# Kernel optimization log

Hardware: AMD Instinct MI355X
Metric: run time of the kernel (lower is better)

## Reference

```python
import jax, jax.numpy as jnp
import numpy as np

N_NODES = 100000
N_EDGES = 1000000
N_GRAPHS = 512
IN_DIM = 3
HID = 64


def setup_inputs() -> dict:
    key = jax.random.key(0)
    ks = jax.random.split(key, 7)
    x = jax.random.normal(ks[0], (N_NODES, IN_DIM), dtype=jnp.float32)
    edge_index = jax.random.randint(ks[1], (2, N_EDGES), 0, N_NODES, dtype=jnp.int64)
    batch = jnp.sort(jax.random.randint(ks[2], (N_NODES,), 0, N_GRAPHS, dtype=jnp.int64))
    # Glorot-ish init for GCNConv linear weights (PyG uses glorot), zero bias.
    W1 = jax.random.normal(ks[3], (IN_DIM, HID), dtype=jnp.float32) / np.float32(np.sqrt(IN_DIM))
    b1 = jnp.zeros((HID,), dtype=jnp.float32)
    W2 = jax.random.normal(ks[4], (HID, HID), dtype=jnp.float32) / np.float32(np.sqrt(HID))
    b2 = jnp.zeros((HID,), dtype=jnp.float32)
    return {"x": x, "W1": W1, "b1": b1, "W2": W2, "b2": b2,
            "edge_index": edge_index, "batch": batch}


def reference(x, W1, b1, W2, b2, edge_index, batch):
    n = x.shape[0]
    loop = jnp.arange(n)
    # GCNConv adds self-loops, then symmetric normalization D^-1/2 (A+I) D^-1/2
    src = jnp.concatenate([edge_index[0], loop])  # [E+N]
    dst = jnp.concatenate([edge_index[1], loop])  # [E+N]
    deg = jax.ops.segment_sum(jnp.ones(dst.shape[0], x.dtype), dst, num_segments=n)
    dinv = jnp.where(deg > 0, jax.lax.rsqrt(deg), 0.0)
    norm = dinv[src] * dinv[dst]  # [E+N]

    def gcn_conv(h, W, b):
        hw = h @ W                       # [N, out] linear first (PyG order)
        msg = hw[src] * norm[:, None]    # gather + scale, [E+N, out]
        agg = jax.ops.segment_sum(msg, dst, num_segments=n)  # scatter-add
        return agg + b

    h = jax.nn.relu(gcn_conv(x, W1, b1))
    h = jax.nn.relu(gcn_conv(h, W2, b2))

    # global_mean_pool over the batch vector
    sums = jax.ops.segment_sum(h, batch, num_segments=N_GRAPHS)          # [G, HID]
    counts = jax.ops.segment_sum(jnp.ones(n, h.dtype), batch, num_segments=N_GRAPHS)
    return sums / jnp.maximum(counts, 1.0)[:, None]
```

## Files before the change

kernel.cpp:

```cpp
#include <hip/hip_runtime.h>

#define HID 64
#define N_GRAPHS_C 512
#define BSHIFT 8
#define NBUCK_MAX 512
#define CAP 3264
#define EPB 4096

typedef unsigned short u16;
typedef unsigned int u32;
typedef unsigned long long u64;

__device__ __forceinline__ float bf2f(u16 u) {
    union { u32 i; float f; } v; v.i = ((u32)u) << 16; return v.f;
}
__device__ __forceinline__ u16 f2bf(float f) {
    union { float f; u32 i; } v; v.f = f;
    u32 x = v.i;
    return (u16)((x + 0x7fffu + ((x >> 16) & 1u)) >> 16);
}


__device__ __forceinline__ int lower_bound(const int* __restrict__ a, int n, int key) {
    int lo = 0, hi = n;
    while (lo < hi) {
        int mid = (lo + hi) >> 1;
        if (a[mid] < key) lo = mid + 1; else hi = mid;
    }
    return lo;
}

__global__ void prep(int* __restrict__ gcursor, const int* __restrict__ batch,
                     int* __restrict__ gstart, int n, int nGraphs) {
    int t = threadIdx.x;
    gcursor[t] = 0;
    for (int g = t; g <= nGraphs; g += 512)
        gstart[g] = lower_bound(batch, n, g);
}


__global__ void bin_pairs(const int* __restrict__ src, const int* __restrict__ dst,
                          int* __restrict__ gcursor, u32* __restrict__ pairs,
                          int nE, int nbuck) {
    __shared__ int lh[NBUCK_MAX];
    __shared__ int lbase[NBUCK_MAX];
    int t = threadIdx.x;
    lh[t] = 0;
    __syncthreads();
    int base = blockIdx.x * EPB;
    u32 pk[8]; int rj[8], bj[8];
    #pragma unroll
    for (int j = 0; j < 8; ++j) {
        int e = base + j * 512 + t;
        if (e < nE) {
            int s = src[e], d = dst[e];
            bj[j] = d >> BSHIFT;
            pk[j] = ((u32)(d & 255) << 17) | (u32)s;
            rj[j] = atomicAdd(&lh[bj[j]], 1);
        } else {
            bj[j] = -1;
        }
    }
    __syncthreads();
    if (t < nbuck) lbase[t] = (lh[t] > 0) ? atomicAdd(&gcursor[t], lh[t]) : 0;
    __syncthreads();
    #pragma unroll
    for (int j = 0; j < 8; ++j) {
        if (bj[j] >= 0) {
            int pos = bj[j] * CAP + lbase[bj[j]] + rj[j];
            pairs[pos] = pk[j];
        }
    }
}

__global__ void build_csr(const u32* __restrict__ pairs, const int* __restrict__ gcursor,
                          int* __restrict__ csr_src, int2* __restrict__ off2,
                          float* __restrict__ dinv, const float* __restrict__ x,
                          float4* __restrict__ xs, u16* __restrict__ A16, int n) {
    __shared__ int hist[256];
    __shared__ int tmp[256];
    int t = threadIdx.x;
    int b = blockIdx.x;
    int pbeg = b * CAP;
    int pend = pbeg + gcursor[b];
    if (t < 256) hist[t] = 0;
    if (b == 0 && t < 32) ((u32*)(A16 + (size_t)n * HID))[t] = 0;
    __syncthreads();
    for (int i = pbeg + t; i < pend; i += 512)
        atomicAdd(&hist[pairs[i] >> 17], 1);
    __syncthreads();
    int v = 0;
    if (t < 256) { v = hist[t]; tmp[t] = v; }
    __syncthreads();
    for (int d = 1; d < 256; d <<= 1) {
        int add = (t >= d && t < 256) ? tmp[t - d] : 0;
        __syncthreads();
        if (t < 256) tmp[t] += add;
        __syncthreads();
    }
    if (t < 256) {
        int e = pbeg + tmp[t] - v;
        int node = (b << BSHIFT) + t;
        if (node < n) {
            float dv = rsqrtf((float)(v + 1));
            off2[node] = make_int2(e, e + v);
            dinv[node] = dv;
            xs[node] = make_float4(x[3*node]*dv, x[3*node+1]*dv, x[3*node+2]*dv, dv);
        }
        hist[t] = e;
    }
    __syncthreads();
    for (int i = pbeg + t; i < pend; i += 512) {
        u32 p = pairs[i];
        int pos = atomicAdd(&hist[p >> 17], 1);
        csr_src[pos] = (int)(p & 0x1FFFFu);
    }
}


__global__ void agg3(const float4* __restrict__ xs, const int* __restrict__ csr_src,
                     const int2* __restrict__ off2, float4* __restrict__ agg4, int n) {
    int node = blockIdx.x * blockDim.x + threadIdx.x;
    if (node >= n) return;
    int2 be = off2[node];
    int beg = be.x, end = be.y;
    float4 self = xs[node];
    float a0 = 0.f, a1 = 0.f, a2 = 0.f;
    for (int k = beg; k < end; k += 8) {
        int e1 = end - 1;
        int idx[8];
        float4 v[8];
        #pragma unroll
        for (int j = 0; j < 8; ++j) idx[j] = csr_src[min(k + j, e1)];
        #pragma unroll
        for (int j = 0; j < 8; ++j) v[j] = xs[idx[j]];
        #pragma unroll
        for (int j = 0; j < 8; ++j) {
            if (k + j < end) { a0 += v[j].x; a1 += v[j].y; a2 += v[j].z; }
        }
    }
    agg4[node] = make_float4(a0 + self.x, a1 + self.y, a2 + self.z, self.w);
}


#define MM2_NODES 32
__global__ void mm2f(const float4* __restrict__ agg4, const float* __restrict__ W1,
                     const float* __restrict__ b1, const float* __restrict__ W2,
                     u16* __restrict__ A16, int n) {
    __shared__ float w[HID * HID];
    __shared__ float h[MM2_NODES * HID];
    __shared__ float dd[MM2_NODES];
    int t = threadIdx.x;
    for (int i = t; i < HID * HID; i += 256) w[i] = W2[i];
    int base = blockIdx.x * MM2_NODES;
    for (int i = t; i < MM2_NODES * HID; i += 256) {
        int node = base + (i >> 6);
        int f = i & 63;
        float hv = 0.0f;
        if (node < n) {
            float4 a = agg4[node];
            float v = (a.x * W1[f] + a.y * W1[HID + f] + a.z * W1[2 * HID + f]) * a.w + b1[f];
            hv = v > 0.0f ? v : 0.0f;
            if (f == 0) dd[i >> 6] = a.w;
        }
        h[i] = hv;
    }
    __syncthreads();
    int f = t & 63, g = t >> 6;
    float acc[8];
    #pragma unroll
    for (int j = 0; j < 8; ++j) acc[j] = 0.0f;
    #pragma unroll 4
    for (int k = 0; k < HID; ++k) {
        float wk = w[k * HID + f];
        #pragma unroll
        for (int j = 0; j < 8; ++j) acc[j] += h[(g * 8 + j) * HID + k] * wk;
    }
    #pragma unroll
    for (int j = 0; j < 8; ++j) {
        int node = base + g * 8 + j;
        if (node < n) A16[(size_t)node * HID + f] = f2bf(acc[j] * dd[g * 8 + j]);
    }
}


__global__ void gather_nodes(const u16* __restrict__ A16, const float* __restrict__ dinv,
                             const int* __restrict__ csr_src, const int2* __restrict__ off2,
                             const float* __restrict__ bias,
                             u16* __restrict__ H16, int n) {
    int t = threadIdx.x;
    int waveq = t >> 4;
    int m = t & 15;
    int qbase = t & 48;
    int node = blockIdx.x * 16 + waveq;
    if (node >= n) return;
    int2 be = off2[node];
    int beg = be.x, end = be.y;
    u64 selfrow = *(const u64*)(A16 + ((size_t)node << 6) + (m << 2));
    u32 slo = (u32)selfrow, shi = (u32)(selfrow >> 32);
    float acc0 = bf2f((u16)(slo & 0xffffu));
    float acc1 = bf2f((u16)(slo >> 16));
    float acc2 = bf2f((u16)(shi & 0xffffu));
    float acc3 = bf2f((u16)(shi >> 16));
    const char* Ab = (const char*)A16;
    u32 laneoff = (u32)(m << 3);
    for (int k = beg; k < end; k += 8) {
        int lim = min(end - k, 8);
        int myIdx = (m < lim) ? csr_src[k + m] : n;
        int ss[8]; u64 rows[8];
        #pragma unroll
        for (int j = 0; j < 8; ++j)
            ss[j] = __shfl(myIdx, qbase + j, 64);
        #pragma unroll
        for (int j = 0; j < 8; ++j)
            rows[j] = *(const u64*)(Ab + (((u32)ss[j] << 7) | laneoff));
        #pragma unroll
        for (int j = 0; j < 8; ++j) {
            u32 lo = (u32)rows[j], hi = (u32)(rows[j] >> 32);
            acc0 += bf2f((u16)(lo & 0xffffu));
            acc1 += bf2f((u16)(lo >> 16));
            acc2 += bf2f((u16)(hi & 0xffffu));
            acc3 += bf2f((u16)(hi >> 16));
        }
    }
    float ddv = dinv[node];
    float4 bb = *(const float4*)(bias + (m << 2));
    float v0 = fmaxf(acc0 * ddv + bb.x, 0.0f);
    float v1 = fmaxf(acc1 * ddv + bb.y, 0.0f);
    float v2 = fmaxf(acc2 * ddv + bb.z, 0.0f);
    float v3 = fmaxf(acc3 * ddv + bb.w, 0.0f);
    u64 outp = (u64)f2bf(v0) | ((u64)f2bf(v1) << 16)
             | ((u64)f2bf(v2) << 32) | ((u64)f2bf(v3) << 48);
    *(u64*)(H16 + ((size_t)node << 6) + (m << 2)) = outp;
}


__global__ void pool_graph(const u16* __restrict__ H16, const int* __restrict__ gstart,
                           float* __restrict__ out, int n) {
    int g = blockIdx.x;
    int t = threadIdx.x;
    int lo = gstart[g];
    int hi = gstart[g + 1];
    int cntN = hi - lo;
    int sid = t >> 4;
    int m = t & 15;
    float a0 = 0.f, a1 = 0.f, a2 = 0.f, a3 = 0.f;
    int i = lo + sid;
    for (; i + 16 < hi; i += 32) {
        u64 r0 = *(const u64*)(H16 + ((size_t)i << 6) + (m << 2));
        u64 r1 = *(const u64*)(H16 + ((size_t)(i + 16) << 6) + (m << 2));
        u32 l0 = (u32)r0, h0 = (u32)(r0 >> 32);
        u32 l1 = (u32)r1, h1 = (u32)(r1 >> 32);
        a0 += bf2f((u16)(l0 & 0xffffu)) + bf2f((u16)(l1 & 0xffffu));
        a1 += bf2f((u16)(l0 >> 16))     + bf2f((u16)(l1 >> 16));
        a2 += bf2f((u16)(h0 & 0xffffu)) + bf2f((u16)(h1 & 0xffffu));
        a3 += bf2f((u16)(h0 >> 16))     + bf2f((u16)(h1 >> 16));
    }
    if (i < hi) {
        u64 r0 = *(const u64*)(H16 + ((size_t)i << 6) + (m << 2));
        u32 l0 = (u32)r0, h0 = (u32)(r0 >> 32);
        a0 += bf2f((u16)(l0 & 0xffffu));
        a1 += bf2f((u16)(l0 >> 16));
        a2 += bf2f((u16)(h0 & 0xffffu));
        a3 += bf2f((u16)(h0 >> 16));
    }
    a0 += __shfl_xor(a0, 16, 64); a0 += __shfl_xor(a0, 32, 64);
    a1 += __shfl_xor(a1, 16, 64); a1 += __shfl_xor(a1, 32, 64);
    a2 += __shfl_xor(a2, 16, 64); a2 += __shfl_xor(a2, 32, 64);
    a3 += __shfl_xor(a3, 16, 64); a3 += __shfl_xor(a3, 32, 64);
    __shared__ float smf[4 * HID];
    int wave = t >> 6, lane = t & 63;
    if (lane < 16) {
        smf[wave * HID + 4 * lane + 0] = a0;
        smf[wave * HID + 4 * lane + 1] = a1;
        smf[wave * HID + 4 * lane + 2] = a2;
        smf[wave * HID + 4 * lane + 3] = a3;
    }
    __syncthreads();
    if (t < HID) {
        float s = smf[t] + smf[HID + t] + smf[2 * HID + t] + smf[3 * HID + t];
        out[(size_t)g * HID + t] = s / fmaxf((float)cntN, 1.0f);
    }
}


extern "C" void kernel_launch(void* const* d_in, const int* in_sizes, int n_in,
                              void* d_out, int out_size, void* d_ws, size_t ws_size,
                              hipStream_t stream) {
    const float* x  = (const float*)d_in[0];
    const float* W1 = (const float*)d_in[1];
    const float* b1 = (const float*)d_in[2];
    const float* W2 = (const float*)d_in[3];
    const float* b2 = (const float*)d_in[4];
    const int*   ei = (const int*)d_in[5];
    const int*   batch = (const int*)d_in[6];

    const int n  = in_sizes[0] / 3;
    const int nE = in_sizes[5] / 2;
    const int* src = ei;
    const int* dst = ei + nE;
    const int nbuck = (n + ((1 << BSHIFT) - 1)) >> BSHIFT;
    const int nGraphs = out_size / HID;

    char* p = (char*)d_ws;
    int*    gcursor = (int*)p;                p += 2048;
    int*    gstart  = (int*)p;                p += 4096;
    int*    csr_src = (int*)p;                p += (size_t)nbuck * CAP * 4;
    int2*   off2    = (int2*)p;               p += (size_t)n * 8;
    float*  dinv    = (float*)p;              p += (size_t)n * 4;
    float4* xs      = (float4*)p;             p += (size_t)n * 16;
    float4* agg4    = (float4*)p;             p += (size_t)n * 16;
    u16*    A16     = (u16*)p;                p += (size_t)(n + 1) * HID * 2;
    u16*    H2      = (u16*)p;                p += (size_t)n * HID * 2;
    u32*    pairs   = (u32*)A16;

    const int BT = 256;
    const int gridNode = (n + BT - 1) / BT;
    const int gridE2   = (nE + EPB - 1) / EPB;
    const int gridMM2  = (n + MM2_NODES - 1) / MM2_NODES;
    const int gridGath = (n + 15) / 16;

    prep<<<1, 512, 0, stream>>>(gcursor, batch, gstart, n, nGraphs);
    bin_pairs<<<gridE2, 512, 0, stream>>>(src, dst, gcursor, pairs, nE, nbuck);
    build_csr<<<nbuck, 512, 0, stream>>>(pairs, gcursor, csr_src, off2, dinv, x, xs, A16, n);

    agg3<<<gridNode, BT, 0, stream>>>(xs, csr_src, off2, agg4, n);
    mm2f<<<gridMM2, BT, 0, stream>>>(agg4, W1, b1, W2, A16, n);

    gather_nodes<<<gridGath, BT, 0, stream>>>(A16, dinv, csr_src, off2, b2, H2, n);

    pool_graph<<<nGraphs, BT, 0, stream>>>(H2, gstart, (float*)d_out, n);
}
```

Before: 168.9 us.

## Split agg3 across thread pairs, widen gather loads, drop prep kernel

```diff
diff --git a/kernel.cpp b/kernel.cpp
--- a/kernel.cpp
+++ b/kernel.cpp
@@ -5,7 +5,7 @@
 #define BSHIFT 8
 #define NBUCK_MAX 512
 #define CAP 3264
-#define EPB 4096
+#define EPB 2048
 
 typedef unsigned short u16;
 typedef unsigned int u32;
@@ -18,24 +18,6 @@
     union { float f; u32 i; } v; v.f = f;
     u32 x = v.i;
     return (u16)((x + 0x7fffu + ((x >> 16) & 1u)) >> 16);
-}
-
-
-__device__ __forceinline__ int lower_bound(const int* __restrict__ a, int n, int key) {
-    int lo = 0, hi = n;
-    while (lo < hi) {
-        int mid = (lo + hi) >> 1;
-        if (a[mid] < key) lo = mid + 1; else hi = mid;
-    }
-    return lo;
-}
-
-__global__ void prep(int* __restrict__ gcursor, const int* __restrict__ batch,
-                     int* __restrict__ gstart, int n, int nGraphs) {
-    int t = threadIdx.x;
-    gcursor[t] = 0;
-    for (int g = t; g <= nGraphs; g += 512)
-        gstart[g] = lower_bound(batch, n, g);
 }
 
 
@@ -48,9 +30,9 @@
     lh[t] = 0;
     __syncthreads();
     int base = blockIdx.x * EPB;
-    u32 pk[8]; int rj[8], bj[8];
+    u32 pk[4]; int rj[4], bj[4];
     #pragma unroll
-    for (int j = 0; j < 8; ++j) {
+    for (int j = 0; j < 4; ++j) {
         int e = base + j * 512 + t;
         if (e < nE) {
             int s = src[e], d = dst[e];
@@ -65,7 +47,7 @@
     if (t < nbuck) lbase[t] = (lh[t] > 0) ? atomicAdd(&gcursor[t], lh[t]) : 0;
     __syncthreads();
     #pragma unroll
-    for (int j = 0; j < 8; ++j) {
+    for (int j = 0; j < 4; ++j) {
         if (bj[j] >= 0) {
             int pos = bj[j] * CAP + lbase[bj[j]] + rj[j];
             pairs[pos] = pk[j];
@@ -120,26 +102,35 @@
 
 __global__ void agg3(const float4* __restrict__ xs, const int* __restrict__ csr_src,
                      const int2* __restrict__ off2, float4* __restrict__ agg4, int n) {
-    int node = blockIdx.x * blockDim.x + threadIdx.x;
+    int tid = blockIdx.x * blockDim.x + threadIdx.x;
+    int node = tid >> 1, half = tid & 1;
     if (node >= n) return;
     int2 be = off2[node];
-    int beg = be.x, end = be.y;
-    float4 self = xs[node];
+    int cnt = be.y - be.x;
+    int mid = be.x + ((cnt + 1) >> 1);
+    int b = half ? mid : be.x;
+    int e = half ? be.y : mid;
     float a0 = 0.f, a1 = 0.f, a2 = 0.f;
-    for (int k = beg; k < end; k += 8) {
-        int e1 = end - 1;
-        int idx[8];
-        float4 v[8];
-        #pragma unroll
-        for (int j = 0; j < 8; ++j) idx[j] = csr_src[min(k + j, e1)];
-        #pragma unroll
-        for (int j = 0; j < 8; ++j) v[j] = xs[idx[j]];
-        #pragma unroll
-        for (int j = 0; j < 8; ++j) {
-            if (k + j < end) { a0 += v[j].x; a1 += v[j].y; a2 += v[j].z; }
-        }
-    }
-    agg4[node] = make_float4(a0 + self.x, a1 + self.y, a2 + self.z, self.w);
+    for (int k = b; k < e; k += 4) {
+        int e1 = e - 1;
+        int idx[4];
+        float4 v[4];
+        #pragma unroll
+        for (int j = 0; j < 4; ++j) idx[j] = csr_src[min(k + j, e1)];
+        #pragma unroll
+        for (int j = 0; j < 4; ++j) v[j] = xs[idx[j]];
+        #pragma unroll
+        for (int j = 0; j < 4; ++j) {
+            if (k + j < e) { a0 += v[j].x; a1 += v[j].y; a2 += v[j].z; }
+        }
+    }
+    a0 += __shfl_xor(a0, 1, 64);
+    a1 += __shfl_xor(a1, 1, 64);
+    a2 += __shfl_xor(a2, 1, 64);
+    if (half == 0) {
+        float4 self = xs[node];
+        agg4[node] = make_float4(a0 + self.x, a1 + self.y, a2 + self.z, self.w);
+    }
 }
 
 
@@ -189,58 +180,77 @@
                              const float* __restrict__ bias,
                              u16* __restrict__ H16, int n) {
     int t = threadIdx.x;
-    int waveq = t >> 4;
-    int m = t & 15;
-    int qbase = t & 48;
-    int node = blockIdx.x * 16 + waveq;
+    int grp = t >> 3;
+    int m = t & 7;
+    int gbase = t & 56;
+    int node = blockIdx.x * 32 + grp;
     if (node >= n) return;
     int2 be = off2[node];
     int beg = be.x, end = be.y;
-    u64 selfrow = *(const u64*)(A16 + ((size_t)node << 6) + (m << 2));
-    u32 slo = (u32)selfrow, shi = (u32)(selfrow >> 32);
-    float acc0 = bf2f((u16)(slo & 0xffffu));
-    float acc1 = bf2f((u16)(slo >> 16));
-    float acc2 = bf2f((u16)(shi & 0xffffu));
-    float acc3 = bf2f((u16)(shi >> 16));
+    uint4 sr = *(const uint4*)(A16 + ((size_t)node << 6) + (m << 3));
+    float acc0 = bf2f((u16)(sr.x & 0xffffu)), acc1 = bf2f((u16)(sr.x >> 16));
+    float acc2 = bf2f((u16)(sr.y & 0xffffu)), acc3 = bf2f((u16)(sr.y >> 16));
+    float acc4 = bf2f((u16)(sr.z & 0xffffu)), acc5 = bf2f((u16)(sr.z >> 16));
+    float acc6 = bf2f((u16)(sr.w & 0xffffu)), acc7 = bf2f((u16)(sr.w >> 16));
     const char* Ab = (const char*)A16;
-    u32 laneoff = (u32)(m << 3);
-    for (int k = beg; k < end; k += 8) {
-        int lim = min(end - k, 8);
-        int myIdx = (m < lim) ? csr_src[k + m] : n;
-        int ss[8]; u64 rows[8];
-        #pragma unroll
-        for (int j = 0; j < 8; ++j)
-            ss[j] = __shfl(myIdx, qbase + j, 64);
-        #pragma unroll
-        for (int j = 0; j < 8; ++j)
-            rows[j] = *(const u64*)(Ab + (((u32)ss[j] << 7) | laneoff));
-        #pragma unroll
-        for (int j = 0; j < 8; ++j) {
-            u32 lo = (u32)rows[j], hi = (u32)(rows[j] >> 32);
-            acc0 += bf2f((u16)(lo & 0xffffu));
-            acc1 += bf2f((u16)(lo >> 16));
-            acc2 += bf2f((u16)(hi & 0xffffu));
-            acc3 += bf2f((u16)(hi >> 16));
+    u32 laneoff = (u32)(m << 4);
+    for (int k = beg; k < end; k += 4) {
+        int lim = end - k;
+        int myIdx = (m < lim && m < 4) ? csr_src[k + m] : n;
+        int ss[4]; uint4 rows[4];
+        #pragma unroll
+        for (int j = 0; j < 4; ++j)
+            ss[j] = __shfl(myIdx, gbase + j, 64);
+        #pragma unroll
+        for (int j = 0; j < 4; ++j)
+            rows[j] = *(const uint4*)(Ab + (((u32)ss[j] << 7) | laneoff));
+        #pragma unroll
+        for (int j = 0; j < 4; ++j) {
+            acc0 += bf2f((u16)(rows[j].x & 0xffffu));
+            acc1 += bf2f((u16)(rows[j].x >> 16));
+            acc2 += bf2f((u16)(rows[j].y & 0xffffu));
+            acc3 += bf2f((u16)(rows[j].y >> 16));
+            acc4 += bf2f((u16)(rows[j].z & 0xffffu));
+            acc5 += bf2f((u16)(rows[j].z >> 16));
+            acc6 += bf2f((u16)(rows[j].w & 0xffffu));
+            acc7 += bf2f((u16)(rows[j].w >> 16));
         }
     }
     float ddv = dinv[node];
-    float4 bb = *(const float4*)(bias + (m << 2));
-    float v0 = fmaxf(acc0 * ddv + bb.x, 0.0f);
-    float v1 = fmaxf(acc1 * ddv + bb.y, 0.0f);
-    float v2 = fmaxf(acc2 * ddv + bb.z, 0.0f);
-    float v3 = fmaxf(acc3 * ddv + bb.w, 0.0f);
-    u64 outp = (u64)f2bf(v0) | ((u64)f2bf(v1) << 16)
-             | ((u64)f2bf(v2) << 32) | ((u64)f2bf(v3) << 48);
-    *(u64*)(H16 + ((size_t)node << 6) + (m << 2)) = outp;
-}
-
-
-__global__ void pool_graph(const u16* __restrict__ H16, const int* __restrict__ gstart,
+    const float4 bb0 = *(const float4*)(bias + (m << 3));
+    const float4 bb1 = *(const float4*)(bias + (m << 3) + 4);
+    float v0 = fmaxf(acc0 * ddv + bb0.x, 0.0f);
+    float v1 = fmaxf(acc1 * ddv + bb0.y, 0.0f);
+    float v2 = fmaxf(acc2 * ddv + bb0.z, 0.0f);
+    float v3 = fmaxf(acc3 * ddv + bb0.w, 0.0f);
+    float v4 = fmaxf(acc4 * ddv + bb1.x, 0.0f);
+    float v5 = fmaxf(acc5 * ddv + bb1.y, 0.0f);
+    float v6 = fmaxf(acc6 * ddv + bb1.z, 0.0f);
+    float v7 = fmaxf(acc7 * ddv + bb1.w, 0.0f);
+    uint4 outp;
+    outp.x = (u32)f2bf(v0) | ((u32)f2bf(v1) << 16);
+    outp.y = (u32)f2bf(v2) | ((u32)f2bf(v3) << 16);
+    outp.z = (u32)f2bf(v4) | ((u32)f2bf(v5) << 16);
+    outp.w = (u32)f2bf(v6) | ((u32)f2bf(v7) << 16);
+    *(uint4*)(H16 + ((size_t)node << 6) + (m << 3)) = outp;
+}
+
+
+__device__ __forceinline__ int lower_bound(const int* __restrict__ a, int n, int key) {
+    int lo = 0, hi = n;
+    while (lo < hi) {
+        int mid = (lo + hi) >> 1;
+        if (a[mid] < key) lo = mid + 1; else hi = mid;
+    }
+    return lo;
+}
+
+__global__ void pool_graph(const u16* __restrict__ H16, const int* __restrict__ batch,
                            float* __restrict__ out, int n) {
     int g = blockIdx.x;
     int t = threadIdx.x;
-    int lo = gstart[g];
-    int hi = gstart[g + 1];
+    int lo = lower_bound(batch, n, g);
+    int hi = lower_bound(batch, n, g + 1);
     int cntN = hi - lo;
     int sid = t >> 4;
     int m = t & 15;
@@ -304,7 +314,6 @@
 
     char* p = (char*)d_ws;
     int*    gcursor = (int*)p;                p += 2048;
-    int*    gstart  = (int*)p;                p += 4096;
     int*    csr_src = (int*)p;                p += (size_t)nbuck * CAP * 4;
     int2*   off2    = (int2*)p;               p += (size_t)n * 8;
     float*  dinv    = (float*)p;              p += (size_t)n * 4;
@@ -315,19 +324,19 @@
     u32*    pairs   = (u32*)A16;
 
     const int BT = 256;
-    const int gridNode = (n + BT - 1) / BT;
     const int gridE2   = (nE + EPB - 1) / EPB;
+    const int gridAgg  = (2 * n + BT - 1) / BT;
     const int gridMM2  = (n + MM2_NODES - 1) / MM2_NODES;
-    const int gridGath = (n + 15) / 16;
-
-    prep<<<1, 512, 0, stream>>>(gcursor, batch, gstart, n, nGraphs);
+    const int gridGath = (n + 31) / 32;
+
+    hipMemsetAsync(gcursor, 0, 2048, stream);
     bin_pairs<<<gridE2, 512, 0, stream>>>(src, dst, gcursor, pairs, nE, nbuck);
     build_csr<<<nbuck, 512, 0, stream>>>(pairs, gcursor, csr_src, off2, dinv, x, xs, A16, n);
 
-    agg3<<<gridNode, BT, 0, stream>>>(xs, csr_src, off2, agg4, n);
+    agg3<<<gridAgg, BT, 0, stream>>>(xs, csr_src, off2, agg4, n);
     mm2f<<<gridMM2, BT, 0, stream>>>(agg4, W1, b1, W2, A16, n);
 
     gather_nodes<<<gridGath, BT, 0, stream>>>(A16, dinv, csr_src, off2, b2, H2, n);
 
-    pool_graph<<<nGraphs, BT, 0, stream>>>(H2, gstart, (float*)d_out, n);
-}
+    pool_graph<<<nGraphs, BT, 0, stream>>>(H2, batch, (float*)d_out, n);
+}
```

After: 169.4 us. Within noise of the previous version (+0.3%).
